# Performance work log

Measured on AMD Instinct MI355X. Metric: run time of the kernel, lower is better.

## Reference

```python
import jax, jax.numpy as jnp
import numpy as np

B, NQ, E, D = 64, 64, 1024, 768
NH, NP = 16, 4
GH = GW = 24
EPS = 1e-5


def _ln(x, g, b):
    m = jnp.mean(x, axis=-1, keepdims=True)
    v = jnp.mean((x - m) ** 2, axis=-1, keepdims=True)
    return (x - m) / jnp.sqrt(v + EPS) * g + b


def _lin_init(k, fan_in, shape_w, shape_b):
    kw, kb = jax.random.split(k)
    s = 1.0 / np.sqrt(fan_in)
    w = jax.random.uniform(kw, shape_w, minval=-s, maxval=s, dtype=jnp.float32)
    b = jax.random.uniform(kb, shape_b, minval=-s, maxval=s, dtype=jnp.float32)
    return w, b


def setup_inputs() -> dict:
    key = jax.random.key(0)
    ks = jax.random.split(key, 16)
    inp = {}
    inp['features'] = jax.random.normal(ks[0], (B, GH * GW, D), dtype=jnp.float32)
    inp['p1_w'], inp['p1_b'] = _lin_init(ks[1], D, (E, D), (E,))
    inp['p2_w'], inp['p2_b'] = _lin_init(ks[2], 4 * D, (E, 4 * D), (E,))
    inp['p3_w'], inp['p3_b'] = _lin_init(ks[3], 9 * D, (E, 9 * D), (E,))
    inp['query_emb'] = jax.random.normal(ks[4], (1, NQ, E), dtype=jnp.float32)
    inp['rg_w1'], inp['rg_b1'] = _lin_init(ks[5], E, (E, E), (E,))
    inp['rg_g'] = jnp.ones((E,), jnp.float32)
    inp['rg_b'] = jnp.zeros((E,), jnp.float32)
    inp['rg_w2'], inp['rg_b2'] = _lin_init(ks[6], E, (2, E), (2,))
    # sampling_offsets: weight init to 0, bias uniform(-0.1, 0.1) per the module
    inp['so_w'] = jnp.zeros((NH * NP * 2, E), jnp.float32)
    inp['so_b'] = jax.random.uniform(ks[7], (NH * NP * 2,), minval=-0.1, maxval=0.1, dtype=jnp.float32)
    inp['aw_w'], inp['aw_b'] = _lin_init(ks[8], E, (NH * NP, E), (NH * NP,))
    inp['vp_w'], inp['vp_b'] = _lin_init(ks[9], E, (E, E), (E,))
    inp['op_w'], inp['op_b'] = _lin_init(ks[10], E, (E, E), (E,))
    inp['fln_g'] = jnp.ones((E,), jnp.float32)
    inp['fln_b'] = jnp.zeros((E,), jnp.float32)
    inp['fin_w'], inp['fin_b'] = _lin_init(ks[11], E, (E, E), (E,))
    return inp


def reference(features, p1_w, p1_b, p2_w, p2_b, p3_w, p3_b, query_emb,
              rg_w1, rg_b1, rg_g, rg_b, rg_w2, rg_b2,
              so_w, so_b, aw_w, aw_b, vp_w, vp_b, op_w, op_b,
              fln_g, fln_b, fin_w, fin_b):
    Bn = features.shape[0]
    hd = E // NH
    x = features.reshape(Bn, GH, GW, D)

    # ---- multi-scale feature extraction (2x2 / 3x3 block concat to match 4D/9D projections) ----
    s1 = features @ p1_w.T + p1_b                                   # [B, GH*GW, E]
    s2in = x.reshape(Bn, GH // 2, 2, GW // 2, 2, D).transpose(0, 1, 3, 2, 4, 5)
    s2 = s2in.reshape(Bn, (GH // 2) * (GW // 2), 4 * D) @ p2_w.T + p2_b
    s3in = x.reshape(Bn, GH // 3, 3, GW // 3, 3, D).transpose(0, 1, 3, 2, 4, 5)
    s3 = s3in.reshape(Bn, (GH // 3) * (GW // 3), 9 * D) @ p3_w.T + p3_b
    levels = [(GH, GW), (GH // 2, GW // 2), (GH // 3, GW // 3)]

    # ---- reference points from learned queries ----
    q = jnp.broadcast_to(query_emb, (Bn, NQ, E))
    h = jax.nn.gelu(_ln(q @ rg_w1.T + rg_b1, rg_g, rg_b), approximate=False)
    rp = jax.nn.sigmoid(h @ rg_w2.T + rg_b2)                        # [B, NQ, 2] in (0,1)

    # ---- deformable attention ----
    value = jnp.concatenate([s1, s2, s3], axis=1) @ vp_w.T + vp_b   # [B, Lv_tot, E]
    value = value.reshape(Bn, -1, NH, hd)
    off = (q @ so_w.T + so_b).reshape(Bn, NQ, NH, NP, 2)
    aw = jax.nn.softmax((q @ aw_w.T + aw_b).reshape(Bn, NQ, NH, NP), axis=-1)

    out = jnp.zeros((Bn, NQ, E), value.dtype)
    start = 0
    for (Hs, Ws) in levels:
        Lv = Hs * Ws
        sp = jnp.clip(rp[:, :, None, None, :] + off, 0.0, 1.0)      # [B, NQ, NH, NP, 2]
        x0 = jnp.floor(sp[..., 0] * (Ws - 1)).astype(jnp.int32)
        y0 = jnp.floor(sp[..., 1] * (Hs - 1)).astype(jnp.int32)
        idx = y0 * Ws + x0                                          # [B, NQ, NH, NP]
        vl = value[:, start:start + Lv].transpose(0, 2, 1, 3)       # [B, NH, Lv, hd]
        idx2 = idx.transpose(0, 2, 1, 3).reshape(Bn, NH, NQ * NP)
        g = jnp.take_along_axis(vl, idx2[..., None], axis=2)        # [B, NH, NQ*NP, hd]
        g = g.reshape(Bn, NH, NQ, NP, hd)
        out = out + jnp.einsum('bhqpd,bqhp->bqhd', g, aw).reshape(Bn, NQ, E)
        start += Lv

    out = out @ op_w.T + op_b
    return _ln(out, fln_g, fln_b) @ fin_w.T + fin_b
```

## Files before the change

### kernel.cpp

```cpp
#include <hip/hip_runtime.h>
#include <math.h>

#define EE 1024
#define ROWS_TOT 784
#define WWN 10752

typedef __attribute__((ext_vector_type(4))) float f4;
typedef __attribute__((ext_vector_type(4))) float f32x4;
typedef __attribute__((ext_vector_type(8))) __bf16 bf16x8;
typedef __attribute__((ext_vector_type(8))) unsigned short ushort8;
typedef __attribute__((ext_vector_type(4))) unsigned short us4;

__device__ __forceinline__ unsigned short f2b(float x) {
    unsigned int u = __float_as_uint(x);
    unsigned int r = (u + 0x7fffu + ((u >> 16) & 1u)) >> 16;
    return (unsigned short)r;
}
__device__ __forceinline__ float b2f(unsigned short u) {
    unsigned int v = ((unsigned int)u) << 16;
    return __uint_as_float(v);
}

#define GLOAD16(g, l) __builtin_amdgcn_global_load_lds( \
    (const __attribute__((address_space(1))) unsigned int*)(g), \
    (__attribute__((address_space(3))) unsigned int*)(l), 16, 0, 0)

template<int MODE, bool SPLIT, int KT>
__device__ __forceinline__ void gemm_body(
    unsigned short* __restrict__ AsB, unsigned short* __restrict__ BsB,
    const unsigned short* __restrict__ FEAT, const unsigned short* __restrict__ WW,
    const float* __restrict__ bias, void* __restrict__ outp,
    int by, int bx, int ktBase)
{
    constexpr int gw = (MODE == 1) ? 24 : (MODE == 2 ? 12 : 8);
    constexpr int Rl = gw * gw;
    constexpr int colOff = (MODE == 1) ? 0 : (MODE == 2 ? 768 : 3840);
    constexpr int rowOff = (MODE == 1) ? 0 : (MODE == 2 ? 576 : 720);

    const int t = threadIdx.x;
    const int lane = t & 63;
    const int w = t >> 6;
    const int wm = w >> 2;
    const int wn = w & 3;
    const int m0 = by * 256, n0 = bx * 256;

    f32x4 acc[8][4] = {};

    const int srow = lane >> 3;
    const int sseg = lane & 7;
    const int sgx  = sseg ^ srow;
    int rbA[4];
#pragma unroll
    for (int g = 0; g < 4; ++g) {
        int gr = m0 + w * 32 + g * 8 + srow;
        if (MODE == 1) rbA[g] = gr;
        else {
            int b_ = gr / Rl, rl = gr - b_ * Rl;
            rbA[g] = b_ * 576 + (MODE * (rl / gw)) * 24 + MODE * (rl % gw);
        }
    }
    const unsigned short* gBbase = WW + (size_t)(n0 + w * 32 + srow) * WWN + colOff + sgx * 8;

    const int fr = lane & 15;
    const int kg = lane >> 4;
    const int kgx0 = kg ^ (fr & 7);
    const int kgx1 = kgx0 ^ 4;
    const int aOff0 = (wm * 128 + fr) * 64 + kgx0 * 8;
    const int aOff1 = (wm * 128 + fr) * 64 + kgx1 * 8;
    const int bOff0 = (wn * 64 + fr) * 64 + kgx0 * 8;
    const int bOff1 = (wn * 64 + fr) * 64 + kgx1 * 8;

    auto STAGE = [&](int buf, int ktl) {
        int kt = ktBase + ktl;
        int s = kt / 12;
        int within = (kt - s * 12) * 64;
        int add = 0;
        if (MODE == 2)      add = (s >> 1) * 24 + (s & 1);
        else if (MODE == 3) { int di = s / 3; add = di * 24 + (s - 3 * di); }
        unsigned short* Asb = AsB + buf * 16384;
        unsigned short* Bsb = BsB + buf * 16384;
#pragma unroll
        for (int g = 0; g < 4; ++g)
            GLOAD16(FEAT + (size_t)(rbA[g] + add) * 768 + within + sgx * 8,
                    Asb + (w * 32 + g * 8) * 64);
#pragma unroll
        for (int g = 0; g < 4; ++g)
            GLOAD16(gBbase + (size_t)(g * 8) * WWN + (size_t)kt * 64,
                    Bsb + (w * 32 + g * 8) * 64);
    };

    int cur = 0;
    STAGE(0, 0);

    for (int tt = 0; tt < KT; ++tt) {
        asm volatile("s_waitcnt vmcnt(0)" ::: "memory");
        __builtin_amdgcn_s_barrier();
        __builtin_amdgcn_sched_barrier(0);

        if (tt + 1 < KT) STAGE(cur ^ 1, tt + 1);
        __builtin_amdgcn_sched_barrier(0);

        const unsigned short* Asc = AsB + cur * 16384;
        const unsigned short* Bsc = BsB + cur * 16384;

        {
            bf16x8 bf[4], af[8];
#pragma unroll
            for (int j = 0; j < 4; ++j) bf[j] = *(const bf16x8*)(Bsc + bOff0 + j * 1024);
#pragma unroll
            for (int i = 0; i < 8; ++i) af[i] = *(const bf16x8*)(Asc + aOff0 + i * 1024);
            __builtin_amdgcn_s_setprio(1);
#pragma unroll
            for (int i = 0; i < 8; ++i)
#pragma unroll
                for (int j = 0; j < 4; ++j)
                    acc[i][j] = __builtin_amdgcn_mfma_f32_16x16x32_bf16(af[i], bf[j], acc[i][j], 0, 0, 0);
            __builtin_amdgcn_s_setprio(0);
        }
        __builtin_amdgcn_s_barrier();
        __builtin_amdgcn_sched_barrier(0);

        {
            bf16x8 bf[4], af[8];
#pragma unroll
            for (int j = 0; j < 4; ++j) bf[j] = *(const bf16x8*)(Bsc + bOff1 + j * 1024);
#pragma unroll
            for (int i = 0; i < 8; ++i) af[i] = *(const bf16x8*)(Asc + aOff1 + i * 1024);
            __builtin_amdgcn_s_setprio(1);
#pragma unroll
            for (int i = 0; i < 8; ++i)
#pragma unroll
                for (int j = 0; j < 4; ++j)
                    acc[i][j] = __builtin_amdgcn_mfma_f32_16x16x32_bf16(af[i], bf[j], acc[i][j], 0, 0, 0);
            __builtin_amdgcn_s_setprio(0);
        }
        cur ^= 1;
    }

#pragma unroll
    for (int i = 0; i < 8; ++i) {
#pragma unroll
        for (int r = 0; r < 4; ++r) {
            int m = m0 + wm * 128 + i * 16 + kg * 4 + r;
#pragma unroll
            for (int j = 0; j < 4; ++j) {
                int n = n0 + wn * 64 + j * 16 + fr;
                if (SPLIT) {
                    ((unsigned short*)outp)[(size_t)m * EE + n] = f2b(acc[i][j][r]);
                } else {
                    int b_o = m / Rl, rl_o = m - b_o * Rl;
                    int crow = b_o * ROWS_TOT + rowOff + rl_o;
                    ((unsigned short*)outp)[(size_t)crow * EE + n] = f2b(acc[i][j][r] + bias[n]);
                }
            }
        }
    }
}

__global__ __launch_bounds__(512, 2) void gemm_val_merged(
    const unsigned short* __restrict__ FEAT, const unsigned short* __restrict__ WW,
    const float* __restrict__ b1, unsigned short* __restrict__ VAL,
    unsigned short* __restrict__ PART2, unsigned short* __restrict__ PART3)
{
    __shared__ unsigned short As[2 * 256 * 64];
    __shared__ unsigned short Bs[2 * 256 * 64];

    int bid = blockIdx.x;
    if (bid < 256) {
        int s = ((bid & 7) << 5) | (bid >> 3);
        int z = s >> 6, r = s & 63;
        gemm_body<3, true, 27>(As, Bs, FEAT, WW, nullptr,
                               PART3 + (size_t)z * 4194304, r >> 2, r & 3, z * 27);
    } else if (bid < 688) {
        int j = bid - 256;
        int s = (j & 7) * 54 + (j >> 3);
        int z = s / 144, r = s - z * 144;
        gemm_body<2, true, 16>(As, Bs, FEAT, WW, nullptr,
                               PART2 + (size_t)z * 9437184, r >> 2, r & 3, z * 16);
    } else {
        int j = bid - 688;
        int s = (j & 7) * 72 + (j >> 3);
        gemm_body<1, false, 12>(As, Bs, FEAT, WW, b1, VAL, s >> 2, s & 3, 0);
    }
}

__global__ void reduce_both_kernel(const unsigned short* __restrict__ P2, const unsigned short* __restrict__ P3,
                                   const float* __restrict__ b2, const float* __restrict__ b3,
                                   unsigned short* __restrict__ VAL)
{
    int blk = blockIdx.x;
    const unsigned short* P;
    const float* bb;
    size_t stride;
    int nsl;
    int isL2 = (blk < 4608);
    if (isL2) { P = P2; bb = b2; stride = 9437184; nsl = 3; }
    else      { P = P3; bb = b3; stride = 4194304; nsl = 4; blk -= 4608; }
    size_t e0 = ((size_t)blk * 256 + threadIdx.x) * 8;
    int m = (int)(e0 >> 10);
    int n = (int)(e0 & 1023);
    float s[8] = {0.f};
    for (int k = 0; k < nsl; ++k) {
        ushort8 a = *(const ushort8*)(P + (size_t)k * stride + e0);
#pragma unroll
        for (int i = 0; i < 8; ++i) s[i] += b2f(a[i]);
    }
    int crow;
    if (isL2) crow = (m / 144) * ROWS_TOT + 576 + (m % 144);
    else      crow = (m >> 6) * ROWS_TOT + 720 + (m & 63);
    ushort8 o;
#pragma unroll
    for (int i = 0; i < 8; ++i) o[i] = f2b(s[i] + bb[n + i]);
    *(ushort8*)(VAL + (size_t)crow * EE + n) = o;
}

template<bool OB>
__global__ __launch_bounds__(256, 2) void gemm2w(
    const unsigned short* __restrict__ A, const unsigned short* __restrict__ Bw,
    const float* __restrict__ bias, void* __restrict__ Cv,
    int M, int N, int K)
{
    __shared__ unsigned short As[2][128 * 64];
    __shared__ unsigned short Bs[2][128 * 64];

    const int t = threadIdx.x;
    const int lane = t & 63;
    const int w = t >> 6;
    const int wm = w >> 1, wn = w & 1;

    int nwg = gridDim.x * gridDim.y;
    int bid = blockIdx.y * gridDim.x + blockIdx.x;
    int chunk = nwg >> 3;
    int swz = (bid & 7) * chunk + (bid >> 3);
    int by = swz / gridDim.x, bx = swz % gridDim.x;
    const int m0 = by * 128, n0 = bx * 128;

    f32x4 acc[4][4] = {};

    const int srow = lane >> 3;
    const int sseg = lane & 7;
    const int sgx  = sseg ^ srow;
    const unsigned short* gA = A + (size_t)(m0 + w * 32 + srow) * K + sgx * 8;
    const unsigned short* gB = Bw + (size_t)(n0 + w * 32 + srow) * K + sgx * 8;

    const int fr = lane & 15;
    const int kg = lane >> 4;
    const int kgx0 = kg ^ (fr & 7);
    const int kgx1 = kgx0 ^ 4;
    const int aOff0 = (wm * 64 + fr) * 64 + kgx0 * 8;
    const int aOff1 = (wm * 64 + fr) * 64 + kgx1 * 8;
    const int bOff0 = (wn * 64 + fr) * 64 + kgx0 * 8;
    const int bOff1 = (wn * 64 + fr) * 64 + kgx1 * 8;

    auto STAGE = [&](int buf, int kt) {
        size_t k0 = (size_t)kt * 64;
#pragma unroll
        for (int g = 0; g < 4; ++g)
            GLOAD16(gA + (size_t)(g * 8) * K + k0, &As[buf][(w * 32 + g * 8) * 64]);
#pragma unroll
        for (int g = 0; g < 4; ++g)
            GLOAD16(gB + (size_t)(g * 8) * K + k0, &Bs[buf][(w * 32 + g * 8) * 64]);
    };

    const int nt = K >> 6;
    int cur = 0;
    STAGE(0, 0);

    for (int tt = 0; tt < nt; ++tt) {
        asm volatile("s_waitcnt vmcnt(0)" ::: "memory");
        __builtin_amdgcn_s_barrier();
        __builtin_amdgcn_sched_barrier(0);

        if (tt + 1 < nt) STAGE(cur ^ 1, tt + 1);
        __builtin_amdgcn_sched_barrier(0);

        {
            bf16x8 bf[4], af[4];
#pragma unroll
            for (int j = 0; j < 4; ++j) bf[j] = *(const bf16x8*)(&Bs[cur][bOff0] + j * 1024);
#pragma unroll
            for (int i = 0; i < 4; ++i) af[i] = *(const bf16x8*)(&As[cur][aOff0] + i * 1024);
            __builtin_amdgcn_s_setprio(1);
#pragma unroll
            for (int i = 0; i < 4; ++i)
#pragma unroll
                for (int j = 0; j < 4; ++j)
                    acc[i][j] = __builtin_amdgcn_mfma_f32_16x16x32_bf16(af[i], bf[j], acc[i][j], 0, 0, 0);
            __builtin_amdgcn_s_setprio(0);
        }
        __builtin_amdgcn_s_barrier();
        __builtin_amdgcn_sched_barrier(0);

        {
            bf16x8 bf[4], af[4];
#pragma unroll
            for (int j = 0; j < 4; ++j) bf[j] = *(const bf16x8*)(&Bs[cur][bOff1] + j * 1024);
#pragma unroll
            for (int i = 0; i < 4; ++i) af[i] = *(const bf16x8*)(&As[cur][aOff1] + i * 1024);
            __builtin_amdgcn_s_setprio(1);
#pragma unroll
            for (int i = 0; i < 4; ++i)
#pragma unroll
                for (int j = 0; j < 4; ++j)
                    acc[i][j] = __builtin_amdgcn_mfma_f32_16x16x32_bf16(af[i], bf[j], acc[i][j], 0, 0, 0);
            __builtin_amdgcn_s_setprio(0);
        }
        cur ^= 1;
    }

#pragma unroll
    for (int i = 0; i < 4; ++i) {
#pragma unroll
        for (int r = 0; r < 4; ++r) {
            int m = m0 + wm * 64 + i * 16 + kg * 4 + r;
#pragma unroll
            for (int j = 0; j < 4; ++j) {
                int n = n0 + wn * 64 + j * 16 + fr;
                float v = acc[i][j][r];
                if (bias) v += bias[n];
                if (OB) ((unsigned short*)Cv)[(size_t)m * N + n] = f2b(v);
                else    ((float*)Cv)[(size_t)m * N + n] = v;
            }
        }
    }
}

__global__ void prep_kernel(const float* __restrict__ feat, unsigned short* __restrict__ FEAT,
                            const float* __restrict__ vpw, unsigned short* __restrict__ VPW,
                            const float* __restrict__ opw, unsigned short* __restrict__ OPW,
                            const float* __restrict__ finw, unsigned short* __restrict__ FINW,
                            const float* __restrict__ p1, const float* __restrict__ p2,
                            const float* __restrict__ p3, unsigned short* __restrict__ PT,
                            const float* __restrict__ vp_b,
                            const float* __restrict__ pb1, const float* __restrict__ pb2,
                            const float* __restrict__ pb3,
                            float* __restrict__ o1, float* __restrict__ o2, float* __restrict__ o3)
{
    __shared__ float tile[32][33];
    int blk = blockIdx.x;
    if (blk < 15360) {
        const float* in; unsigned short* out;
        if (blk < 13824)       { in = feat; out = FEAT; }
        else if (blk < 14336)  { in = vpw;  out = VPW;  blk -= 13824; }
        else if (blk < 14848)  { in = opw;  out = OPW;  blk -= 14336; }
        else                   { in = finw; out = FINW; blk -= 14848; }
        size_t i = ((size_t)blk * 256 + threadIdx.x) * 8;
        f4 x = *(const f4*)(in + i);
        f4 y = *(const f4*)(in + i + 4);
        ushort8 o;
        o[0] = f2b(x[0]); o[1] = f2b(x[1]); o[2] = f2b(x[2]); o[3] = f2b(x[3]);
        o[4] = f2b(y[0]); o[5] = f2b(y[1]); o[6] = f2b(y[2]); o[7] = f2b(y[3]);
        *(ushort8*)(out + i) = o;
    } else if (blk < 26112) {
        int fl = blk - 15360;
        int bx = fl % 336, byy = fl / 336;
        const float* in; unsigned short* out; int C;
        if (bx < 24)       { in = p1; out = PT;                C = 768; }
        else if (bx < 120) { in = p2; out = PT + 768  * 1024;  C = 3072; bx -= 24; }
        else               { in = p3; out = PT + 3840 * 1024;  C = 6912; bx -= 120; }
        const int R = 1024;
        int c0 = bx * 32, r0 = byy * 32;
        int tx = threadIdx.x & 31, ty = threadIdx.x >> 5;
#pragma unroll
        for (int i = 0; i < 32; i += 8)
            tile[ty + i][tx] = in[(size_t)(r0 + ty + i) * C + c0 + tx];
        __syncthreads();
#pragma unroll
        for (int i = 0; i < 32; i += 8)
            out[(size_t)(c0 + ty + i) * R + r0 + tx] = f2b(tile[tx][ty + i]);
    } else {
        int b = blk - 26112;
        const float* pb; float* bout;
        if (b < 256)      { pb = pb1; bout = o1; }
        else if (b < 512) { pb = pb2; bout = o2; b -= 256; }
        else              { pb = pb3; bout = o3; b -= 512; }
        int e = b * 4 + (threadIdx.x >> 6);
        int lane = threadIdx.x & 63;
        float s = 0.f;
        for (int k = lane; k < EE; k += 64) s += vpw[(size_t)e * EE + k] * pb[k];
#pragma unroll
        for (int o = 32; o > 0; o >>= 1) s += __shfl_down(s, o, 64);
        if (lane == 0) bout[e] = s + vp_b[e];
    }
}

__global__ void rg1_kernel(const float* __restrict__ qe, const float* __restrict__ w,
                           const float* __restrict__ b, double* __restrict__ h0)
{
    int o = blockIdx.x * 4 + (threadIdx.x >> 6);
    int lane = threadIdx.x & 63;
    int q = o >> 10, n = o & 1023;
    double s = 0.0;
    for (int k = lane; k < EE; k += 64)
        s += (double)qe[q * EE + k] * (double)w[(size_t)n * EE + k];
#pragma unroll
    for (int off = 32; off > 0; off >>= 1) s += __shfl_down(s, off, 64);
    if (lane == 0) h0[o] = s + (double)b[n];
}

__global__ void ln_gelu_rp_kernel(const double* __restrict__ h0, const float* __restrict__ g,
                                  const float* __restrict__ bb, const float* __restrict__ w2,
                                  const float* __restrict__ b2, double* __restrict__ rp)
{
    __shared__ double red[256];
    __shared__ double stats[2];
    __shared__ double hsh[1024];
    int q = blockIdx.x, t = threadIdx.x;
    double x[4];
#pragma unroll
    for (int i = 0; i < 4; ++i) x[i] = h0[q * 1024 + t + i * 256];
    double s = x[0] + x[1] + x[2] + x[3];
    red[t] = s; __syncthreads();
    for (int o = 128; o; o >>= 1) { if (t < o) red[t] += red[t + o]; __syncthreads(); }
    if (t == 0) stats[0] = red[0] / 1024.0;
    __syncthreads();
    double mean = stats[0];
    double d = 0.0;
#pragma unroll
    for (int i = 0; i < 4; ++i) { double dd = x[i] - mean; d += dd * dd; }
    red[t] = d; __syncthreads();
    for (int o = 128; o; o >>= 1) { if (t < o) red[t] += red[t + o]; __syncthreads(); }
    if (t == 0) stats[1] = red[0] / 1024.0;
    __syncthreads();
    double inv = 1.0 / sqrt(stats[1] + 1e-5);
#pragma unroll
    for (int i = 0; i < 4; ++i) {
        int c = t + i * 256;
        double y = (x[i] - mean) * inv * (double)g[c] + (double)bb[c];
        hsh[c] = y * 0.5 * (1.0 + erf(y * 0.70710678118654752440));
    }
    __syncthreads();
    if (t < 128) {
        int r = t >> 6;
        int lane = t & 63;
        double sv = 0.0;
        for (int k = lane; k < EE; k += 64)
            sv += hsh[k] * (double)w2[r * 1024 + k];
#pragma unroll
        for (int off = 32; off > 0; off >>= 1) sv += __shfl_down(sv, off, 64);
        if (lane == 0) rp[q * 2 + r] = 1.0 / (1.0 + exp(-(sv + (double)b2[r])));
    }
}

__global__ void offlog_kernel(const float* __restrict__ qe, const float* __restrict__ so_w,
                              const float* __restrict__ so_b, const float* __restrict__ aw_w,
                              const float* __restrict__ aw_b,
                              double* __restrict__ offv_g, double* __restrict__ logit_g)
{
    int o = blockIdx.x * 4 + (threadIdx.x >> 6);
    int lane = threadIdx.x & 63;
    const float* wrow;
    double bias;
    int q;
    if (o < 8192) { q = o >> 7; int j = o & 127; wrow = so_w + (size_t)j * EE; bias = (double)so_b[j]; }
    else          { int r = o - 8192; q = r >> 6; int n = r & 63; wrow = aw_w + (size_t)n * EE; bias = (double)aw_b[n]; }
    double s = 0.0;
    for (int k = lane; k < EE; k += 64)
        s += (double)qe[q * EE + k] * (double)wrow[k];
#pragma unroll
    for (int off = 32; off > 0; off >>= 1) s += __shfl_down(s, off, 64);
    if (lane == 0) {
        if (o < 8192) offv_g[o] = s + bias;
        else          logit_g[o - 8192] = s + bias;
    }
}

__global__ void offfin_kernel(const double* __restrict__ offv_g, const double* __restrict__ logit_g,
                              const double* __restrict__ rp,
                              float* __restrict__ awf, int* __restrict__ idxv)
{
    int q = blockIdx.x, t = threadIdx.x;
    int hh = t >> 2, p = t & 3;
    const double* logit = logit_g + q * 64;
    const double* offv  = offv_g + q * 128;
    double l0 = logit[hh * 4 + 0], l1 = logit[hh * 4 + 1];
    double l2 = logit[hh * 4 + 2], l3 = logit[hh * 4 + 3];
    double m = fmax(fmax(l0, l1), fmax(l2, l3));
    double den = exp(l0 - m) + exp(l1 - m) + exp(l2 - m) + exp(l3 - m);
    awf[(q * 16 + hh) * 4 + p] = (float)(exp(logit[hh * 4 + p] - m) / den);
    const int Wss[3] = {24, 12, 8};
    const int starts[3] = {0, 576, 720};
    double ox = offv[(hh * 4 + p) * 2 + 0], oy = offv[(hh * 4 + p) * 2 + 1];
    double rx = rp[q * 2 + 0], ry = rp[q * 2 + 1];
#pragma unroll
    for (int l = 0; l < 3; ++l) {
        int Ws = Wss[l];
        double sx = rx + ox; sx = sx < 0.0 ? 0.0 : (sx > 1.0 ? 1.0 : sx);
        double sy = ry + oy; sy = sy < 0.0 ? 0.0 : (sy > 1.0 ? 1.0 : sy);
        int x0 = (int)floor(sx * (double)(Ws - 1));
        int y0 = (int)floor(sy * (double)(Ws - 1));
        idxv[((l * 64 + q) * 16 + hh) * 4 + p] = starts[l] + y0 * Ws + x0;
    }
}

__global__ void gather_kernel(const unsigned short* __restrict__ value, const float* __restrict__ awf,
                              const int* __restrict__ idxv, unsigned short* __restrict__ out0)
{
    int idx = blockIdx.x * 256 + threadIdx.x;
    int d8 = idx & 7;
    int h  = (idx >> 3) & 15;
    int bq = idx >> 7;
    int b  = bq >> 6, q = bq & 63;
    float s[8] = {0.f};
#pragma unroll
    for (int l = 0; l < 3; ++l)
#pragma unroll
        for (int p = 0; p < 4; ++p) {
            int row = idxv[((l * 64 + q) * 16 + h) * 4 + p];
            float wgt = awf[(q * 16 + h) * 4 + p];
            ushort8 v = *(const ushort8*)(value + ((size_t)(b * ROWS_TOT + row)) * 1024 + h * 64 + d8 * 8);
#pragma unroll
            for (int i = 0; i < 8; ++i) s[i] += wgt * b2f(v[i]);
        }
    ushort8 o;
#pragma unroll
    for (int i = 0; i < 8; ++i) o[i] = f2b(s[i]);
    *(ushort8*)(out0 + (size_t)bq * 1024 + h * 64 + d8 * 8) = o;
}

__global__ void ln_b2b_kernel(const unsigned short* __restrict__ x, const float* __restrict__ g,
                              const float* __restrict__ bb, unsigned short* __restrict__ y)
{
    __shared__ float red[256];
    __shared__ float stats[2];
    int r = blockIdx.x, t = threadIdx.x;
    us4 v4 = *(const us4*)(x + (size_t)r * 1024 + t * 4);
    float v[4];
#pragma unroll
    for (int i = 0; i < 4; ++i) v[i] = b2f(v4[i]);
    float s = v[0] + v[1] + v[2] + v[3];
    red[t] = s; __syncthreads();
    for (int o = 128; o; o >>= 1) { if (t < o) red[t] += red[t + o]; __syncthreads(); }
    if (t == 0) stats[0] = red[0] / 1024.f;
    __syncthreads();
    float mean = stats[0];
    float d = 0.f;
#pragma unroll
    for (int i = 0; i < 4; ++i) { float dd = v[i] - mean; d += dd * dd; }
    red[t] = d; __syncthreads();
    for (int o = 128; o; o >>= 1) { if (t < o) red[t] += red[t + o]; __syncthreads(); }
    if (t == 0) stats[1] = red[0] / 1024.f;
    __syncthreads();
    float inv = 1.f / sqrtf(stats[1] + 1e-5f);
    us4 o4;
#pragma unroll
    for (int i = 0; i < 4; ++i) {
        int c = t * 4 + i;
        o4[i] = f2b((v[i] - mean) * inv * g[c] + bb[c]);
    }
    *(us4*)(y + (size_t)r * 1024 + t * 4) = o4;
}

extern "C" void kernel_launch(void* const* d_in, const int* in_sizes, int n_in,
                              void* d_out, int out_size, void* d_ws, size_t ws_size,
                              hipStream_t stream)
{
    const float* features  = (const float*)d_in[0];
    const float* p1_w      = (const float*)d_in[1];
    const float* p1_b      = (const float*)d_in[2];
    const float* p2_w      = (const float*)d_in[3];
    const float* p2_b      = (const float*)d_in[4];
    const float* p3_w      = (const float*)d_in[5];
    const float* p3_b      = (const float*)d_in[6];
    const float* query_emb = (const float*)d_in[7];
    const float* rg_w1     = (const float*)d_in[8];
    const float* rg_b1     = (const float*)d_in[9];
    const float* rg_g      = (const float*)d_in[10];
    const float* rg_b      = (const float*)d_in[11];
    const float* rg_w2     = (const float*)d_in[12];
    const float* rg_b2     = (const float*)d_in[13];
    const float* so_w      = (const float*)d_in[14];
    const float* so_b      = (const float*)d_in[15];
    const float* aw_w      = (const float*)d_in[16];
    const float* aw_b      = (const float*)d_in[17];
    const float* vp_w      = (const float*)d_in[18];
    const float* vp_b      = (const float*)d_in[19];
    const float* op_w      = (const float*)d_in[20];
    const float* op_b      = (const float*)d_in[21];
    const float* fln_g     = (const float*)d_in[22];
    const float* fln_b     = (const float*)d_in[23];
    const float* fin_w     = (const float*)d_in[24];
    const float* fin_b     = (const float*)d_in[25];
    float* out = (float*)d_out;

    char* p = (char*)d_ws;
    unsigned short* FEAT = (unsigned short*)p; p += 56623104;
    unsigned short* PT   = (unsigned short*)p; p += 22020096;
    unsigned short* WW   = (unsigned short*)p; p += 22020096;
    unsigned short* VPW  = (unsigned short*)p; p += 2097152;
    unsigned short* VAL  = (unsigned short*)p; p += 102760448;
    unsigned short* PART = (unsigned short*)p; p += 75497472;
    unsigned short* OPO  = (unsigned short*)p; p += 8388608;
    unsigned short* OUT0 = (unsigned short*)p; p += 8388608;
    unsigned short* LNO  = (unsigned short*)p; p += 8388608;
    unsigned short* OPW  = (unsigned short*)p; p += 2097152;
    unsigned short* FINW = (unsigned short*)p; p += 2097152;
    float* b1p  = (float*)p; p += 4096;
    float* b2p  = (float*)p; p += 4096;
    float* b3p  = (float*)p; p += 4096;
    float* awf  = (float*)p; p += 16384;
    int*   idxv = (int*)p;   p += 49152;
    double* h0  = (double*)p; p += 524288;
    double* rp  = (double*)p; p += 1024;
    double* offv_g  = (double*)p; p += 65536;
    double* logit_g = (double*)p; p += 32768;

    dim3 blk(256);

    rg1_kernel<<<16384, blk, 0, stream>>>(query_emb, rg_w1, rg_b1, h0);
    ln_gelu_rp_kernel<<<64, blk, 0, stream>>>(h0, rg_g, rg_b, rg_w2, rg_b2, rp);
    offlog_kernel<<<3072, blk, 0, stream>>>(query_emb, so_w, so_b, aw_w, aw_b, offv_g, logit_g);
    offfin_kernel<<<64, 64, 0, stream>>>(offv_g, logit_g, rp, awf, idxv);

    prep_kernel<<<26880, blk, 0, stream>>>(features, FEAT, vp_w, VPW, op_w, OPW, fin_w, FINW,
                                           p1_w, p2_w, p3_w, PT,
                                           vp_b, p1_b, p2_b, p3_b, b1p, b2p, b3p);

    gemm2w<true><<<dim3(84, 8), blk, 0, stream>>>(VPW, PT, nullptr, WW, 1024, WWN, 1024);

    gemm_val_merged<<<1264, 512, 0, stream>>>(FEAT, WW, b1p, VAL, PART, PART + 3 * 9437184);
    reduce_both_kernel<<<6656, blk, 0, stream>>>(PART, PART + 3 * 9437184, b2p, b3p, VAL);

    gather_kernel<<<2048, blk, 0, stream>>>(VAL, awf, idxv, OUT0);

    gemm2w<true><<<dim3(8, 32), blk, 0, stream>>>(OUT0, OPW, op_b, OPO, 4096, 1024, 1024);
    ln_b2b_kernel<<<4096, blk, 0, stream>>>(OPO, fln_g, fln_b, LNO);
    gemm2w<false><<<dim3(8, 32), blk, 0, stream>>>(LNO, FINW, fin_b, out, 4096, 1024, 1024);
}
```

Measured before the change: 462.0 us.

## Fuse split-K partial reduction into gather and cut level-2 split count

Removes the separate reduce kernel that summed split-K partials for levels 2 and 3 into the value buffer. The gather now reads the partial slices only at the sampled rows and adds the biases there. Level 2 also drops from 3 to 2 K-slices (24 k-tiles each), which shrinks the GEMM grid and the partial buffer. This avoids a full pass that reads and writes the partials, at the cost of fewer parallel blocks for level 2 and more loads per gathered sample.

```diff
diff --git a/kernel.cpp b/kernel.cpp
--- a/kernel.cpp
+++ b/kernel.cpp
@@ -171,47 +171,80 @@
         int z = s >> 6, r = s & 63;
         gemm_body<3, true, 27>(As, Bs, FEAT, WW, nullptr,
                                PART3 + (size_t)z * 4194304, r >> 2, r & 3, z * 27);
-    } else if (bid < 688) {
+    } else if (bid < 544) {
         int j = bid - 256;
-        int s = (j & 7) * 54 + (j >> 3);
+        int s = (j & 7) * 36 + (j >> 3);
         int z = s / 144, r = s - z * 144;
-        gemm_body<2, true, 16>(As, Bs, FEAT, WW, nullptr,
-                               PART2 + (size_t)z * 9437184, r >> 2, r & 3, z * 16);
+        gemm_body<2, true, 24>(As, Bs, FEAT, WW, nullptr,
+                               PART2 + (size_t)z * 9437184, r >> 2, r & 3, z * 24);
     } else {
-        int j = bid - 688;
+        int j = bid - 544;
         int s = (j & 7) * 72 + (j >> 3);
         gemm_body<1, false, 12>(As, Bs, FEAT, WW, b1, VAL, s >> 2, s & 3, 0);
     }
 }
 
-__global__ void reduce_both_kernel(const unsigned short* __restrict__ P2, const unsigned short* __restrict__ P3,
-                                   const float* __restrict__ b2, const float* __restrict__ b3,
-                                   unsigned short* __restrict__ VAL)
-{
-    int blk = blockIdx.x;
-    const unsigned short* P;
-    const float* bb;
-    size_t stride;
-    int nsl;
-    int isL2 = (blk < 4608);
-    if (isL2) { P = P2; bb = b2; stride = 9437184; nsl = 3; }
-    else      { P = P3; bb = b3; stride = 4194304; nsl = 4; blk -= 4608; }
-    size_t e0 = ((size_t)blk * 256 + threadIdx.x) * 8;
-    int m = (int)(e0 >> 10);
-    int n = (int)(e0 & 1023);
+__global__ void gather_fused_kernel(const unsigned short* __restrict__ VAL,
+                                    const unsigned short* __restrict__ P2,
+                                    const unsigned short* __restrict__ P3,
+                                    const float* __restrict__ b2, const float* __restrict__ b3,
+                                    const float* __restrict__ awf, const int* __restrict__ idxv,
+                                    unsigned short* __restrict__ out0)
+{
+    int idx = blockIdx.x * 256 + threadIdx.x;
+    int d8 = idx & 7;
+    int h  = (idx >> 3) & 15;
+    int bq = idx >> 7;
+    int b  = bq >> 6, q = bq & 63;
+    int n0 = h * 64 + d8 * 8;
     float s[8] = {0.f};
-    for (int k = 0; k < nsl; ++k) {
-        ushort8 a = *(const ushort8*)(P + (size_t)k * stride + e0);
-#pragma unroll
-        for (int i = 0; i < 8; ++i) s[i] += b2f(a[i]);
-    }
-    int crow;
-    if (isL2) crow = (m / 144) * ROWS_TOT + 576 + (m % 144);
-    else      crow = (m >> 6) * ROWS_TOT + 720 + (m & 63);
+
+#pragma unroll
+    for (int p = 0; p < 4; ++p) {
+        int row = idxv[((0 * 64 + q) * 16 + h) * 4 + p];
+        float wgt = awf[(q * 16 + h) * 4 + p];
+        ushort8 v = *(const ushort8*)(VAL + ((size_t)(b * ROWS_TOT + row)) * 1024 + n0);
+#pragma unroll
+        for (int i = 0; i < 8; ++i) s[i] += wgt * b2f(v[i]);
+    }
+
+    float bias2[8];
+#pragma unroll
+    for (int i = 0; i < 8; ++i) bias2[i] = b2[n0 + i];
+#pragma unroll
+    for (int p = 0; p < 4; ++p) {
+        int rl = idxv[((1 * 64 + q) * 16 + h) * 4 + p] - 576;
+        float wgt = awf[(q * 16 + h) * 4 + p];
+        size_t mo = ((size_t)(b * 144 + rl)) * 1024 + n0;
+        ushort8 va = *(const ushort8*)(P2 + mo);
+        ushort8 vb = *(const ushort8*)(P2 + 9437184 + mo);
+#pragma unroll
+        for (int i = 0; i < 8; ++i) s[i] += wgt * (b2f(va[i]) + b2f(vb[i]) + bias2[i]);
+    }
+
+    float bias3[8];
+#pragma unroll
+    for (int i = 0; i < 8; ++i) bias3[i] = b3[n0 + i];
+#pragma unroll
+    for (int p = 0; p < 4; ++p) {
+        int rl = idxv[((2 * 64 + q) * 16 + h) * 4 + p] - 720;
+        float wgt = awf[(q * 16 + h) * 4 + p];
+        size_t mo = ((size_t)(b * 64 + rl)) * 1024 + n0;
+        float a8[8] = {0.f};
+#pragma unroll
+        for (int k = 0; k < 4; ++k) {
+            ushort8 v = *(const ushort8*)(P3 + (size_t)k * 4194304 + mo);
+#pragma unroll
+            for (int i = 0; i < 8; ++i) a8[i] += b2f(v[i]);
+        }
+#pragma unroll
+        for (int i = 0; i < 8; ++i) s[i] += wgt * (a8[i] + bias3[i]);
+    }
+
     ushort8 o;
 #pragma unroll
-    for (int i = 0; i < 8; ++i) o[i] = f2b(s[i] + bb[n + i]);
-    *(ushort8*)(VAL + (size_t)crow * EE + n) = o;
+    for (int i = 0; i < 8; ++i) o[i] = f2b(s[i]);
+    *(ushort8*)(out0 + (size_t)bq * 1024 + n0) = o;
 }
 
 template<bool OB>
@@ -491,31 +524,6 @@
         int y0 = (int)floor(sy * (double)(Ws - 1));
         idxv[((l * 64 + q) * 16 + hh) * 4 + p] = starts[l] + y0 * Ws + x0;
     }
-}
-
-__global__ void gather_kernel(const unsigned short* __restrict__ value, const float* __restrict__ awf,
-                              const int* __restrict__ idxv, unsigned short* __restrict__ out0)
-{
-    int idx = blockIdx.x * 256 + threadIdx.x;
-    int d8 = idx & 7;
-    int h  = (idx >> 3) & 15;
-    int bq = idx >> 7;
-    int b  = bq >> 6, q = bq & 63;
-    float s[8] = {0.f};
-#pragma unroll
-    for (int l = 0; l < 3; ++l)
-#pragma unroll
-        for (int p = 0; p < 4; ++p) {
-            int row = idxv[((l * 64 + q) * 16 + h) * 4 + p];
-            float wgt = awf[(q * 16 + h) * 4 + p];
-            ushort8 v = *(const ushort8*)(value + ((size_t)(b * ROWS_TOT + row)) * 1024 + h * 64 + d8 * 8);
-#pragma unroll
-            for (int i = 0; i < 8; ++i) s[i] += wgt * b2f(v[i]);
-        }
-    ushort8 o;
-#pragma unroll
-    for (int i = 0; i < 8; ++i) o[i] = f2b(s[i]);
-    *(ushort8*)(out0 + (size_t)bq * 1024 + h * 64 + d8 * 8) = o;
 }
 
 __global__ void ln_b2b_kernel(const unsigned short* __restrict__ x, const float* __restrict__ g,
@@ -589,7 +597,7 @@
     unsigned short* WW   = (unsigned short*)p; p += 22020096;
     unsigned short* VPW  = (unsigned short*)p; p += 2097152;
     unsigned short* VAL  = (unsigned short*)p; p += 102760448;
-    unsigned short* PART = (unsigned short*)p; p += 75497472;
+    unsigned short* PART = (unsigned short*)p; p += 71303168;
     unsigned short* OPO  = (unsigned short*)p; p += 8388608;
     unsigned short* OUT0 = (unsigned short*)p; p += 8388608;
     unsigned short* LNO  = (unsigned short*)p; p += 8388608;
@@ -605,6 +613,9 @@
     double* offv_g  = (double*)p; p += 65536;
     double* logit_g = (double*)p; p += 32768;
 
+    unsigned short* PART2 = PART;
+    unsigned short* PART3 = PART + 2 * 9437184;
+
     dim3 blk(256);
 
     rg1_kernel<<<16384, blk, 0, stream>>>(query_emb, rg_w1, rg_b1, h0);
@@ -618,10 +629,9 @@
 
     gemm2w<true><<<dim3(84, 8), blk, 0, stream>>>(VPW, PT, nullptr, WW, 1024, WWN, 1024);
 
-    gemm_val_merged<<<1264, 512, 0, stream>>>(FEAT, WW, b1p, VAL, PART, PART + 3 * 9437184);
-    reduce_both_kernel<<<6656, blk, 0, stream>>>(PART, PART + 3 * 9437184, b2p, b3p, VAL);
-
-    gather_kernel<<<2048, blk, 0, stream>>>(VAL, awf, idxv, OUT0);
+    gemm_val_merged<<<1120, 512, 0, stream>>>(FEAT, WW, b1p, VAL, PART2, PART3);
+
+    gather_fused_kernel<<<2048, blk, 0, stream>>>(VAL, PART2, PART3, b2p, b3p, awf, idxv, OUT0);
 
     gemm2w<true><<<dim3(8, 32), blk, 0, stream>>>(OUT0, OPW, op_b, OPO, 4096, 1024, 1024);
     ln_b2b_kernel<<<4096, blk, 0, stream>>>(OPO, fln_g, fln_b, LNO);
```

Result: no change. 455.5 us (-1.4%).
